# Optimization experiments

Hardware: AMD Instinct MI355X
Metric: run time of the kernel (lower is better)

Reference implementation:

```python
import math
import jax, jax.numpy as jnp
import numpy as np

B, D, N, K = 16, 512, 2048, 32  # batch, latent_dim, n points, k feature width


def setup_inputs() -> dict:
    key = jax.random.key(0)
    ks = jax.random.split(key, 11)
    s = 0.02
    return {
        "x": jax.random.normal(ks[0], (B, D), jnp.float32),
        "WQ": jax.random.normal(ks[1], (D, N * K), jnp.float32) * s,
        "bQ": jax.random.normal(ks[2], (N * K,), jnp.float32) * s,
        "WK": jax.random.normal(ks[3], (D, N * K), jnp.float32) * s,
        "bK": jax.random.normal(ks[4], (N * K,), jnp.float32) * s,
        "WV": jax.random.normal(ks[5], (D, N * K), jnp.float32) * s,
        "bV": jax.random.normal(ks[6], (N * K,), jnp.float32) * s,
        "Wout": jax.random.normal(ks[7], (3, K), jnp.float32) * s,
        "bout": jax.random.normal(ks[8], (3,), jnp.float32) * s,
        "Wori": jax.random.normal(ks[9], (3, K), jnp.float32) * s,
        "bori": jax.random.normal(ks[10], (3,), jnp.float32) * s,
    }


def reference(x, WQ, bQ, WK, bK, WV, bV, Wout, bout, Wori, bori):
    b = x.shape[0]
    q = (x @ WQ + bQ).reshape(b, N, K)   # fc_Q output, used for both Q and ori
    k = (x @ WK + bK).reshape(b, N, K)
    v = (x @ WV + bV).reshape(b, N, K)
    # conv_ori is a pointwise Conv1d(K, 3, 1) applied to ori^T -> [b,3,N];
    # computed in [b,N,3] layout (final output layout after the last transpose).
    ori = jnp.einsum('bnk,ck->bnc', q, Wori) + bori  # [b, N, 3]
    # single-head scaled dot-product attention, scores [b, N, N]
    scores = jnp.einsum('bnk,bmk->bnm', q, k) / math.sqrt(K)
    attn = jax.nn.softmax(scores, axis=2)
    out = jnp.einsum('bnm,bmk->bnk', attn, v)        # [b, N, K]
    out = jnp.einsum('bnk,ck->bnc', out, Wout) + bout  # pointwise conv_output
    return out + ori                                 # [b, N, 3]
```

## Files before the change

### kernel.cpp

```cpp
#include <hip/hip_runtime.h>
#include <hip/hip_bf16.h>
#include <math.h>

#define NB 16
#define ND 512
#define NN 2048
#define NKF 32
#define NNK 65536

typedef short s8v __attribute__((ext_vector_type(8)));
typedef float f4v __attribute__((ext_vector_type(4)));
typedef float f2v __attribute__((ext_vector_type(2)));
typedef unsigned short u16;
typedef unsigned int u32;
typedef u16 u16x8 __attribute__((ext_vector_type(8)));
typedef u32 u32x4 __attribute__((ext_vector_type(4)));

__device__ __forceinline__ u16 f2bf(float x) {
    u32 u = __builtin_bit_cast(u32, x);
    return (u16)((u + 0x7fffu + ((u >> 16) & 1u)) >> 16);
}
__device__ __forceinline__ float bf2f(u16 b) {
    u32 u = ((u32)b) << 16;
    return __builtin_bit_cast(float, u);
}

__global__ __launch_bounds__(256) void proj_partial(
    const float* __restrict__ x,
    const float* __restrict__ WQ, const float* __restrict__ WK,
    const float* __restrict__ WV, u16* __restrict__ part)
{
    const int t = threadIdx.x;
    const int jb = blockIdx.x;
    const int mat = blockIdx.y;
    const int dz = blockIdx.z;
    const float* __restrict__ W = (mat == 0) ? WQ : (mat == 1) ? WK : WV;
    const int j = jb * 512 + t * 2;
    const int d0 = dz * 128;

    f2v acc[16];
    #pragma unroll
    for (int b = 0; b < 16; b++) acc[b] = (f2v){0.f, 0.f};

    const float* wp = W + (size_t)d0 * NNK + j;
    const float* xp = x + d0;

    f2v wa[8], wb[8];
    #pragma unroll
    for (int u = 0; u < 8; u++)
        wa[u] = __builtin_nontemporal_load((const f2v*)(wp + (size_t)u * NNK));

    #pragma unroll 1
    for (int dd = 0; dd < 128; dd += 16) {
        #pragma unroll
        for (int u = 0; u < 8; u++)
            wb[u] = __builtin_nontemporal_load(
                (const f2v*)(wp + (size_t)(dd + 8 + u) * NNK));
        __builtin_amdgcn_sched_barrier(0);

        #pragma unroll
        for (int u = 0; u < 8; u++) {
            const float* xr = xp + dd + u;
            #pragma unroll
            for (int b = 0; b < 16; b++) {
                float xv = xr[b * ND];
                acc[b][0] = fmaf(xv, wa[u][0], acc[b][0]);
                acc[b][1] = fmaf(xv, wa[u][1], acc[b][1]);
            }
        }

        if (dd + 16 < 128) {
            #pragma unroll
            for (int u = 0; u < 8; u++)
                wa[u] = __builtin_nontemporal_load(
                    (const f2v*)(wp + (size_t)(dd + 16 + u) * NNK));
        }
        __builtin_amdgcn_sched_barrier(0);

        #pragma unroll
        for (int u = 0; u < 8; u++) {
            const float* xr = xp + dd + 8 + u;
            #pragma unroll
            for (int b = 0; b < 16; b++) {
                float xv = xr[b * ND];
                acc[b][0] = fmaf(xv, wb[u][0], acc[b][0]);
                acc[b][1] = fmaf(xv, wb[u][1], acc[b][1]);
            }
        }
    }

    size_t base = ((size_t)(mat * 4 + dz) * 16) * NNK + j;
    #pragma unroll
    for (int b = 0; b < 16; b++) {
        u32 pv = (u32)f2bf(acc[b][0]) | ((u32)f2bf(acc[b][1]) << 16);
        *(u32*)(part + base + (size_t)b * NNK) = pv;
    }
}

__global__ __launch_bounds__(256) void reduce_cast(
    const u16* __restrict__ part,
    const float* __restrict__ bQ, const float* __restrict__ bK,
    const float* __restrict__ bV,
    u16* __restrict__ qb, u16* __restrict__ kb, u16* __restrict__ vT)
{
    const int t = threadIdx.x;
    const int bid = blockIdx.x;
    const int xcd = bid & 7;
    const int m = bid >> 3;
    const int b = xcd + 8 * (m >= 96);
    const int r = (m >= 96) ? m - 96 : m;
    const int mat = r >> 5;
    const int jc = r & 31;
    const float* __restrict__ bias = (mat == 0) ? bQ : (mat == 1) ? bK : bV;
    const int j = jc * 2048 + t * 8;

    float4 b0 = *(const float4*)(bias + j);
    float4 b1 = *(const float4*)(bias + j + 4);
    float v[8] = {b0.x, b0.y, b0.z, b0.w, b1.x, b1.y, b1.z, b1.w};

    #pragma unroll
    for (int dz = 0; dz < 4; dz++) {
        size_t p = ((size_t)(mat * 4 + dz) * 16 + b) * NNK + j;
        u16x8 pp = *(const u16x8*)(part + p);
        #pragma unroll
        for (int i = 0; i < 8; i++) v[i] += bf2f(pp[i]);
    }

    const float scale = (mat == 1) ? 0.2550868230023389f : 1.0f;
    u16 h[8];
    #pragma unroll
    for (int i = 0; i < 8; i++) h[i] = f2bf(v[i] * scale);

    __shared__ u16 vt[32][72];

    if (mat < 2) {
        u16* dst = ((mat == 0) ? qb : kb) + (size_t)b * NNK + j;
        u16x8 hv;
        #pragma unroll
        for (int i = 0; i < 8; i++) hv[i] = h[i];
        *(u16x8*)dst = hv;
    } else {
        const int n  = t >> 2;
        const int k0 = (t & 3) * 8;
        #pragma unroll
        for (int i = 0; i < 8; i++) vt[k0 + i][n] = h[i];
        __syncthreads();
        const int k  = t >> 3;
        const int c8 = t & 7;
        u16x8 ov;
        #pragma unroll
        for (int i = 0; i < 8; i++) ov[i] = vt[k][c8 * 8 + i];
        u16* dst = vT + (size_t)b * NNK + (size_t)k * NN + jc * 64 + c8 * 8;
        *(u16x8*)dst = ov;
    }
}

__global__ __launch_bounds__(256) void attn_kernel(
    const u16* __restrict__ qb, const u16* __restrict__ kb,
    const u16* __restrict__ vT,
    const float* __restrict__ Wout, const float* __restrict__ bout,
    const float* __restrict__ Wori, const float* __restrict__ bori,
    float* __restrict__ out)
{
    const int t = threadIdx.x;
    const int w = t >> 6;
    const int l = t & 63;
    const int g = l >> 4;
    const int n = l & 15;
    const int bid = blockIdx.x;
    const int xcd = bid & 7;
    const int m = bid >> 3;
    const int b = xcd + 8 * (m >= 32);
    const int qt = (m >= 32) ? m - 32 : m;
    const int q0 = qt * 64;

    __shared__ __align__(16) u32 Pt[4][16][36];

    const u16* qrow = qb + (size_t)b * NNK + (size_t)(q0 + w * 16 + n) * NKF + g * 8;
    const s8v qf = *(const s8v*)qrow;

    const u16* kbase = kb + (size_t)b * NNK + (size_t)n * NKF + g * 8;
    auto loadK = [&](s8v (&ka)[4], int it) {
        #pragma unroll
        for (int tt = 0; tt < 4; tt++)
            ka[tt] = *(const s8v*)(kbase + (size_t)it * 2048 + tt * 512);
    };
    const u16* vbase0 = vT + (size_t)b * NNK + (size_t)n * NN + g * 8;
    const u16* vbase1 = vT + (size_t)b * NNK + (size_t)(n + 16) * NN + g * 8;
    auto loadV = [&](s8v (&vf)[4], int it) {
        const int off = it * 64;
        vf[0] = *(const s8v*)(vbase0 + off);
        vf[1] = *(const s8v*)(vbase0 + off + 32);
        vf[2] = *(const s8v*)(vbase1 + off);
        vf[3] = *(const s8v*)(vbase1 + off + 32);
    };

    s8v ka0[4], ka1[4], vf0[4], vf1[4];
    loadK(ka0, 0);
    loadV(vf0, 0);

    float lsum = 0.f;
    f4v O0 = {0.f, 0.f, 0.f, 0.f}, O1 = {0.f, 0.f, 0.f, 0.f};

    auto body = [&](s8v (&kc_)[4], s8v (&kn_)[4],
                    s8v (&vc_)[4], s8v (&vn_)[4], int it) {
        if (it + 1 < 32) {
            loadK(kn_, it + 1);
            loadV(vn_, it + 1);
        }

        f4v S[4];
        #pragma unroll
        for (int tt = 0; tt < 4; tt++) {
            f4v z = {0.f, 0.f, 0.f, 0.f};
            S[tt] = __builtin_amdgcn_mfma_f32_16x16x32_bf16(kc_[tt], qf, z, 0, 0, 0);
        }

        float p[4][4];
        #pragma unroll
        for (int tt = 0; tt < 4; tt++)
            #pragma unroll
            for (int r = 0; r < 4; r++) {
                p[tt][r] = exp2f(S[tt][r]);
                lsum += p[tt][r];
            }

        #pragma unroll
        for (int tt = 0; tt < 4; tt++) {
            u32 w0 = (u32)f2bf(p[tt][0]) | ((u32)f2bf(p[tt][1]) << 16);
            u32 w1 = (u32)f2bf(p[tt][2]) | ((u32)f2bf(p[tt][3]) << 16);
            *(uint2*)&Pt[w][n][8 * tt + 2 * g] = make_uint2(w0, w1);
        }

        #pragma unroll
        for (int kc = 0; kc < 2; kc++) {
            u32x4 pw = *(const u32x4*)&Pt[w][n][16 * kc + 4 * g];
            s8v pa = __builtin_bit_cast(s8v, pw);
            O0 = __builtin_amdgcn_mfma_f32_16x16x32_bf16(vc_[kc], pa, O0, 0, 0, 0);
            O1 = __builtin_amdgcn_mfma_f32_16x16x32_bf16(vc_[2 + kc], pa, O1, 0, 0, 0);
        }
    };

    #pragma unroll 1
    for (int i2 = 0; i2 < 16; i2++) {
        body(ka0, ka1, vf0, vf1, 2 * i2);
        body(ka1, ka0, vf1, vf0, 2 * i2 + 1);
    }

    float l_run = lsum;
    l_run += __shfl_xor(l_run, 16);
    l_run += __shfl_xor(l_run, 32);
    const float inv = 1.0f / l_run;

    float po[3] = {0.f, 0.f, 0.f};
    #pragma unroll
    for (int r = 0; r < 4; r++) {
        int dk0 = 4 * g + r;
        int dk1 = 16 + 4 * g + r;
        float o0 = O0[r] * inv;
        float o1 = O1[r] * inv;
        #pragma unroll
        for (int c = 0; c < 3; c++) {
            po[c] += o0 * Wout[c * NKF + dk0];
            po[c] += o1 * Wout[c * NKF + dk1];
        }
    }
    #pragma unroll
    for (int e = 0; e < 8; e++) {
        float qv = bf2f((u16)qf[e]);
        int k = 8 * g + e;
        #pragma unroll
        for (int c = 0; c < 3; c++) po[c] += qv * Wori[c * NKF + k];
    }
    #pragma unroll
    for (int c = 0; c < 3; c++) {
        po[c] += __shfl_xor(po[c], 16);
        po[c] += __shfl_xor(po[c], 32);
    }
    if (g == 0) {
        int row = q0 + w * 16 + n;
        size_t o = ((size_t)b * NN + row) * 3;
        #pragma unroll
        for (int c = 0; c < 3; c++) out[o + c] = po[c] + bout[c] + bori[c];
    }
}

extern "C" void kernel_launch(void* const* d_in, const int* in_sizes, int n_in,
                              void* d_out, int out_size, void* d_ws, size_t ws_size,
                              hipStream_t stream) {
    const float* x    = (const float*)d_in[0];
    const float* WQ   = (const float*)d_in[1];
    const float* bQ   = (const float*)d_in[2];
    const float* WK   = (const float*)d_in[3];
    const float* bK   = (const float*)d_in[4];
    const float* WV   = (const float*)d_in[5];
    const float* bV   = (const float*)d_in[6];
    const float* Wout = (const float*)d_in[7];
    const float* bout = (const float*)d_in[8];
    const float* Wori = (const float*)d_in[9];
    const float* bori = (const float*)d_in[10];
    float* out = (float*)d_out;

    char* ws = (char*)d_ws;
    u16* part = (u16*)ws;
    u16* qb = (u16*)(ws + 25165824);
    u16* kb = (u16*)(ws + 25165824 + 2097152);
    u16* vT = (u16*)(ws + 25165824 + 2 * 2097152);

    proj_partial<<<dim3(128, 3, 4), 256, 0, stream>>>(x, WQ, WK, WV, part);
    reduce_cast<<<dim3(1536), 256, 0, stream>>>(part, bQ, bK, bV, qb, kb, vT);
    attn_kernel<<<dim3(512), 256, 0, stream>>>(qb, kb, vT, Wout, bout, Wori, bori, out);
}
```

Before: 140.9 us.

## Split attention key range across two wave groups per block and combine

Doubles the attention block to 512 threads. Each of the two halves of four waves processes half of the 2048 keys for the same 64 queries. The second half writes its partial O accumulators and row sum to shared memory, and the first half adds them before normalising and running the output projection. This is meant to raise wave-level parallelism and latency hiding on the serial key loop, at the cost of extra shared memory, a block-wide barrier, and higher register pressure under the 512-thread launch bound.

```diff
diff --git a/kernel.cpp b/kernel.cpp
--- a/kernel.cpp
+++ b/kernel.cpp
@@ -155,7 +155,7 @@
     }
 }
 
-__global__ __launch_bounds__(256) void attn_kernel(
+__global__ __launch_bounds__(512) void attn_kernel(
     const u16* __restrict__ qb, const u16* __restrict__ kb,
     const u16* __restrict__ vT,
     const float* __restrict__ Wout, const float* __restrict__ bout,
@@ -163,7 +163,9 @@
     float* __restrict__ out)
 {
     const int t = threadIdx.x;
-    const int w = t >> 6;
+    const int w8 = t >> 6;
+    const int wq = w8 & 3;
+    const int half = w8 >> 2;
     const int l = t & 63;
     const int g = l >> 4;
     const int n = l & 15;
@@ -174,19 +176,20 @@
     const int qt = (m >= 32) ? m - 32 : m;
     const int q0 = qt * 64;
 
-    __shared__ __align__(16) u32 Pt[4][16][36];
-
-    const u16* qrow = qb + (size_t)b * NNK + (size_t)(q0 + w * 16 + n) * NKF + g * 8;
+    __shared__ __align__(16) u32 Pt[8][16][36];
+    __shared__ __align__(16) float Oc[4][64][10];
+
+    const u16* qrow = qb + (size_t)b * NNK + (size_t)(q0 + wq * 16 + n) * NKF + g * 8;
     const s8v qf = *(const s8v*)qrow;
 
-    const u16* kbase = kb + (size_t)b * NNK + (size_t)n * NKF + g * 8;
+    const u16* kbase = kb + (size_t)b * NNK + (size_t)(half * 1024 + n) * NKF + g * 8;
     auto loadK = [&](s8v (&ka)[4], int it) {
         #pragma unroll
         for (int tt = 0; tt < 4; tt++)
             ka[tt] = *(const s8v*)(kbase + (size_t)it * 2048 + tt * 512);
     };
-    const u16* vbase0 = vT + (size_t)b * NNK + (size_t)n * NN + g * 8;
-    const u16* vbase1 = vT + (size_t)b * NNK + (size_t)(n + 16) * NN + g * 8;
+    const u16* vbase0 = vT + (size_t)b * NNK + (size_t)n * NN + half * 1024 + g * 8;
+    const u16* vbase1 = vT + (size_t)b * NNK + (size_t)(n + 16) * NN + half * 1024 + g * 8;
     auto loadV = [&](s8v (&vf)[4], int it) {
         const int off = it * 64;
         vf[0] = *(const s8v*)(vbase0 + off);
@@ -204,7 +207,7 @@
 
     auto body = [&](s8v (&kc_)[4], s8v (&kn_)[4],
                     s8v (&vc_)[4], s8v (&vn_)[4], int it) {
-        if (it + 1 < 32) {
+        if (it + 1 < 16) {
             loadK(kn_, it + 1);
             loadV(vn_, it + 1);
         }
@@ -229,12 +232,12 @@
         for (int tt = 0; tt < 4; tt++) {
             u32 w0 = (u32)f2bf(p[tt][0]) | ((u32)f2bf(p[tt][1]) << 16);
             u32 w1 = (u32)f2bf(p[tt][2]) | ((u32)f2bf(p[tt][3]) << 16);
-            *(uint2*)&Pt[w][n][8 * tt + 2 * g] = make_uint2(w0, w1);
+            *(uint2*)&Pt[w8][n][8 * tt + 2 * g] = make_uint2(w0, w1);
         }
 
         #pragma unroll
         for (int kc = 0; kc < 2; kc++) {
-            u32x4 pw = *(const u32x4*)&Pt[w][n][16 * kc + 4 * g];
+            u32x4 pw = *(const u32x4*)&Pt[w8][n][16 * kc + 4 * g];
             s8v pa = __builtin_bit_cast(s8v, pw);
             O0 = __builtin_amdgcn_mfma_f32_16x16x32_bf16(vc_[kc], pa, O0, 0, 0, 0);
             O1 = __builtin_amdgcn_mfma_f32_16x16x32_bf16(vc_[2 + kc], pa, O1, 0, 0, 0);
@@ -242,10 +245,28 @@
     };
 
     #pragma unroll 1
-    for (int i2 = 0; i2 < 16; i2++) {
+    for (int i2 = 0; i2 < 8; i2++) {
         body(ka0, ka1, vf0, vf1, 2 * i2);
         body(ka1, ka0, vf1, vf0, 2 * i2 + 1);
     }
+
+    if (half == 1) {
+        #pragma unroll
+        for (int r = 0; r < 4; r++) {
+            Oc[wq][l][r] = O0[r];
+            Oc[wq][l][4 + r] = O1[r];
+        }
+        Oc[wq][l][8] = lsum;
+    }
+    __syncthreads();
+    if (half == 1) return;
+
+    #pragma unroll
+    for (int r = 0; r < 4; r++) {
+        O0[r] += Oc[wq][l][r];
+        O1[r] += Oc[wq][l][4 + r];
+    }
+    lsum += Oc[wq][l][8];
 
     float l_run = lsum;
     l_run += __shfl_xor(l_run, 16);
@@ -278,7 +299,7 @@
         po[c] += __shfl_xor(po[c], 32);
     }
     if (g == 0) {
-        int row = q0 + w * 16 + n;
+        int row = q0 + wq * 16 + n;
         size_t o = ((size_t)b * NN + row) * 3;
         #pragma unroll
         for (int c = 0; c < 3; c++) out[o + c] = po[c] + bout[c] + bori[c];
@@ -309,5 +330,5 @@
 
     proj_partial<<<dim3(128, 3, 4), 256, 0, stream>>>(x, WQ, WK, WV, part);
     reduce_cast<<<dim3(1536), 256, 0, stream>>>(part, bQ, bK, bV, qb, kb, vT);
-    attn_kernel<<<dim3(512), 256, 0, stream>>>(qb, kb, vT, Wout, bout, Wori, bori, out);
-}
+    attn_kernel<<<dim3(512), 512, 0, stream>>>(qb, kb, vT, Wout, bout, Wori, bori, out);
+}
```

Result: faster. 135.8 us (-3.6%).
